# Performance work log

Measured on AMD Instinct MI355X. Metric: run time of the kernel, lower is better.

Reference implementation:

```python
import jax, jax.numpy as jnp
import numpy as np

A = 15                    # num_anchor_per_point
H = W = 34                # hardcoded feature map size in the torch module
STRIDE = 16               # heat_map_a
ANCHOR_W = jnp.array([45.3, 32.0, 22.6, 90.5, 64.0, 45.3, 181.0, 128.0, 90.5, 271.5, 192.0, 135.8, 362.0, 256.0, 181.0], dtype=jnp.float32)
ANCHOR_H = jnp.array([22.6, 32.0, 45.3, 45.3, 64.0, 90.5, 90.5, 128.0, 181.0, 135.8, 192.0, 271.5, 181.0, 256.0, 362.0], dtype=jnp.float32)
THRESH_OBJ = 0.2
MIN_H = 6.0
MIN_W = 6.0
MAX_CAND = 5000
TOP_N = 300
OVERLAP = 0.7


def _generate_anchors():
    xmins = -0.5 * (ANCHOR_W - 1.0)
    xmaxs = 0.5 * (ANCHOR_W - 1.0)
    ymins = -0.5 * (ANCHOR_H - 1.0)
    ymaxs = 0.5 * (ANCHOR_H - 1.0)
    return jnp.stack([xmins, ymins, xmaxs, ymaxs], axis=1)  # [A,4]


def _bbox_transform_inv(boxes, deltas):
    widths = boxes[:, 2] - boxes[:, 0] + 1.0
    heights = boxes[:, 3] - boxes[:, 1] + 1.0
    ctr_x = boxes[:, 0] + 0.5 * (widths - 1.0)
    ctr_y = boxes[:, 1] + 0.5 * (heights - 1.0)
    pred_ctr_x = deltas[:, 0] * widths + ctr_x
    pred_ctr_y = deltas[:, 1] * heights + ctr_y
    pred_w = jnp.exp(deltas[:, 2]) * widths
    pred_h = jnp.exp(deltas[:, 3]) * heights
    return jnp.stack([
        pred_ctr_x - 0.5 * (pred_w - 1.0),
        pred_ctr_y - 0.5 * (pred_h - 1.0),
        pred_ctr_x + 0.5 * (pred_w - 1.0),
        pred_ctr_y + 0.5 * (pred_h - 1.0),
    ], axis=1)


def _nms_keep(boxes, valid, thresh):
    # greedy NMS on score-descending boxes; +1 pixel convention matches module
    x1, y1, x2, y2 = boxes[:, 0], boxes[:, 1], boxes[:, 2], boxes[:, 3]
    areas = (x2 - x1 + 1.0) * (y2 - y1 + 1.0)
    iw = jnp.clip(jnp.minimum(x2[:, None], x2[None, :]) - jnp.maximum(x1[:, None], x1[None, :]) + 1.0, 0.0)
    ih = jnp.clip(jnp.minimum(y2[:, None], y2[None, :]) - jnp.maximum(y1[:, None], y1[None, :]) + 1.0, 0.0)
    inter = iw * ih
    iou = inter / (areas[:, None] + areas[None, :] - inter)  # [M,M]
    M = boxes.shape[0]
    idx = jnp.arange(M)

    def body(i, suppressed):
        alive = jnp.logical_not(suppressed[i])
        return suppressed | (alive & (iou[i] > thresh) & (idx > i))

    suppressed = jax.lax.fori_loop(0, M, body, jnp.logical_not(valid))
    return jnp.logical_not(suppressed) & valid


def _forward(rpn_cls_prob_reshape, rpn_bbox_pred, im_info, bbox_mean, bbox_std):
    origin_height = im_info[0].astype(jnp.float32)
    origin_width = im_info[1].astype(jnp.float32)

    # shifts (replicates torch meshgrid indexing='ij' and (y,x,y,x) column order)
    shift_x = jnp.arange(W, dtype=jnp.float32) * STRIDE
    shift_y = jnp.arange(H, dtype=jnp.float32) * STRIDE
    sx, sy = jnp.meshgrid(shift_x, shift_y, indexing='ij')  # [W,H]
    shifts = jnp.stack([sy.ravel(), sx.ravel(), sy.ravel(), sx.ravel()], axis=1)  # [W*H,4]
    anchors = (_generate_anchors()[None, :, :] + shifts[:, None, :]).reshape(-1, 4)  # [W*H*A,4]

    # deltas: [1,4A,34,34] -> (A,4,34,34) -> (34,34,A,4) -> (-1,4)
    deltas = rpn_bbox_pred.reshape(A, 4, H, W).transpose(2, 3, 0, 1).reshape(-1, 4)
    deltas = deltas * bbox_std + bbox_mean
    proposals = _bbox_transform_inv(anchors, deltas)

    # clip to image (refine_out_of_map_bbox=True)
    xs = jnp.clip(proposals[:, 0::2], 0.0, origin_width - 1.0)
    ys = jnp.clip(proposals[:, 1::2], 0.0, origin_height - 1.0)
    proposals = jnp.stack([xs[:, 0], ys[:, 0], xs[:, 1], ys[:, 1]], axis=1)

    # scores: [1,2A,34,34] -> (2,A,HW) -> (HW,A,2) -> (-1,2)
    scores = rpn_cls_prob_reshape.reshape(2, A, -1).transpose(2, 1, 0).reshape(-1, 2)

    # filter (HEIGHT_AND_WIDTH) via masking (jit-friendly, same selected set)
    ws = proposals[:, 2] - proposals[:, 0] + 1.0
    hs = proposals[:, 3] - proposals[:, 1] + 1.0
    keep = (scores[:, 1] > THRESH_OBJ) & (ws >= MIN_W) & (hs >= MIN_H)

    masked_score = jnp.where(keep, scores[:, 1], -1.0)
    top_vals, top_idx = jax.lax.top_k(masked_score, MAX_CAND)  # sorted descending
    cand = proposals[top_idx]
    valid = keep[top_idx]

    kept = _nms_keep(cand, valid, OVERLAP)

    # emit first TOP_N kept boxes in score order, zero-padded, with batch-id col 0
    rank = jnp.cumsum(kept.astype(jnp.int32)) - 1
    dest = jnp.where(kept & (rank < TOP_N), rank, TOP_N)
    out = jnp.zeros((TOP_N + 1, 5), dtype=cand.dtype)
    out = out.at[dest, 1:].set(cand)
    return out[:TOP_N]


def setup_inputs() -> dict:
    key = jax.random.key(0)
    k1, k2 = jax.random.split(key)
    rpn_cls_prob_reshape = jax.random.uniform(k1, (1, 2 * A, H, W), dtype=jnp.float32)
    rpn_bbox_pred = jax.random.normal(k2, (1, 4 * A, H, W), dtype=jnp.float32)
    im_info = jnp.array([544, 544], dtype=jnp.int32)
    bbox_mean = jnp.array([0.0, 0.0, 0.0, 0.0], dtype=jnp.float32)
    bbox_std = jnp.array([0.1, 0.1, 0.2, 0.2], dtype=jnp.float32)
    return {"rpn_cls_prob_reshape": rpn_cls_prob_reshape, "rpn_bbox_pred": rpn_bbox_pred,
            "im_info": im_info, "bbox_mean": bbox_mean, "bbox_std": bbox_std}


def reference(rpn_cls_prob_reshape, rpn_bbox_pred, im_info, bbox_mean, bbox_std):
    return _forward(rpn_cls_prob_reshape, rpn_bbox_pred, im_info, bbox_mean, bbox_std)
```

## Files before the change

kernel.cpp:

```cpp
#include <hip/hip_runtime.h>

#define NA 15
#define GH 34
#define GW 34
#define SP (GH*GW)
#define NB (SP*NA)
#define MAXC 5000
#define TOPN 300
#define NW 80
#define NRALLOC 5056
#define THRESH_OBJ 0.2f
#define NMS_T 0.7f
#define SH 12
#define BLO 0x3E4CCu
#define NBUCK 5120

typedef unsigned long long u64;
typedef unsigned int u32;
struct __align__(16) U2 { u64 x, y; };

__constant__ float c_aw[NA] = {45.3f,32.0f,22.6f,90.5f,64.0f,45.3f,181.0f,128.0f,90.5f,271.5f,192.0f,135.8f,362.0f,256.0f,181.0f};
__constant__ float c_ah[NA] = {22.6f,32.0f,45.3f,45.3f,64.0f,90.5f,90.5f,128.0f,181.0f,135.8f,192.0f,271.5f,181.0f,256.0f,362.0f};

__global__ __launch_bounds__(256) void k_decode(
    const float* __restrict__ cls, const float* __restrict__ pred,
    const int* __restrict__ iminfo, const float* __restrict__ mean,
    const float* __restrict__ stdv, float* __restrict__ boxes,
    u32* __restrict__ sbits) {
#pragma clang fp contract(off)
  int r = blockIdx.x * 256 + threadIdx.x;
  if (r >= NB) return;
  int n = r % NA;
  int p = r / NA;
  int w = p % GW;
  int h = p / GW;

  float score = cls[(NA + n) * SP + p];

  float d0 = pred[(n*4+0)*SP + p] * stdv[0] + mean[0];
  float d1 = pred[(n*4+1)*SP + p] * stdv[1] + mean[1];
  float d2 = pred[(n*4+2)*SP + p] * stdv[2] + mean[2];
  float d3 = pred[(n*4+3)*SP + p] * stdv[3] + mean[3];

  float aw = c_aw[n], ah = c_ah[n];
  float sx = (float)(w * 16);
  float sy = (float)(h * 16);
  float xmin = -0.5f * (aw - 1.0f) + sx;
  float ymin = -0.5f * (ah - 1.0f) + sy;
  float xmax =  0.5f * (aw - 1.0f) + sx;
  float ymax =  0.5f * (ah - 1.0f) + sy;

  float widths  = xmax - xmin + 1.0f;
  float heights = ymax - ymin + 1.0f;
  float ctrx = xmin + 0.5f * (widths - 1.0f);
  float ctry = ymin + 0.5f * (heights - 1.0f);

  float pcx = d0 * widths + ctrx;
  float pcy = d1 * heights + ctry;
  float pw = expf(d2) * widths;
  float ph = expf(d3) * heights;

  float x1 = pcx - 0.5f * (pw - 1.0f);
  float y1 = pcy - 0.5f * (ph - 1.0f);
  float x2 = pcx + 0.5f * (pw - 1.0f);
  float y2 = pcy + 0.5f * (ph - 1.0f);

  float ow = (float)iminfo[1] - 1.0f;
  float oh = (float)iminfo[0] - 1.0f;
  x1 = fminf(fmaxf(x1, 0.0f), ow);
  x2 = fminf(fmaxf(x2, 0.0f), ow);
  y1 = fminf(fmaxf(y1, 0.0f), oh);
  y2 = fminf(fmaxf(y2, 0.0f), oh);

  float ws = x2 - x1 + 1.0f;
  float hs = y2 - y1 + 1.0f;
  bool keep = (score > THRESH_OBJ) && (ws >= 6.0f) && (hs >= 6.0f);

  boxes[r*4+0] = x1;
  boxes[r*4+1] = y1;
  boxes[r*4+2] = x2;
  boxes[r*4+3] = y2;
  sbits[r] = keep ? __float_as_uint(score) : 0u;
}

__global__ __launch_bounds__(1024) void k_bucket(const u32* __restrict__ sbits,
    int* __restrict__ base, int* __restrict__ cnt, u64* __restrict__ blist) {
  __shared__ int sh[NBUCK];
  __shared__ int fl[NBUCK];
  __shared__ int ch[1024];
  int tid = threadIdx.x;
  for (int j = tid; j < NBUCK; j += 1024) { sh[j] = 0; fl[j] = 0; }
  __syncthreads();
  for (int j = tid; j < NB; j += 1024) {
    u32 bits = sbits[j];
    if (bits) { int b = min((int)((bits >> SH) - BLO), NBUCK - 1); atomicAdd(&sh[b], 1); }
  }
  __syncthreads();
  int c0 = sh[tid*5+0], c1 = sh[tid*5+1], c2 = sh[tid*5+2], c3 = sh[tid*5+3], c4 = sh[tid*5+4];
  ch[tid] = c0 + c1 + c2 + c3 + c4;
  __syncthreads();
  for (int off = 1; off < 1024; off <<= 1) {
    int v = ch[tid];
    int u = (tid + off < 1024) ? ch[tid + off] : 0;
    __syncthreads();
    ch[tid] = v + u;
    __syncthreads();
  }
  int S = (tid + 1 < 1024) ? ch[tid + 1] : 0;
  int b4v = S;
  int b3v = b4v + c4;
  int b2v = b3v + c3;
  int b1v = b2v + c2;
  int b0v = b1v + c1;
  base[tid*5+0] = b0v; base[tid*5+1] = b1v; base[tid*5+2] = b2v;
  base[tid*5+3] = b3v; base[tid*5+4] = b4v;
  sh[tid*5+0] = b0v; sh[tid*5+1] = b1v; sh[tid*5+2] = b2v;
  sh[tid*5+3] = b3v; sh[tid*5+4] = b4v;
  if (tid == 0) *cnt = ch[0];
  __syncthreads();
  for (int j = tid; j < NB; j += 1024) {
    u32 bits = sbits[j];
    if (!bits) continue;
    int b = min((int)((bits >> SH) - BLO), NBUCK - 1);
    int pos = sh[b] + atomicAdd(&fl[b], 1);
    blist[pos] = ((u64)bits << 32) | (u64)(0xFFFFFFFFu - (u32)j);
  }
}

__global__ __launch_bounds__(256) void k_final(const u32* __restrict__ sbits,
    const int* __restrict__ base, const int* __restrict__ cnt,
    const u64* __restrict__ blist, const float* __restrict__ boxes,
    float* __restrict__ sboxes) {
  int i = blockIdx.x * 256 + threadIdx.x;
  if (i >= NB) return;
  u32 bits = sbits[i];
  if (!bits) return;
  int b = min((int)((bits >> SH) - BLO), NBUCK - 1);
  u64 key = ((u64)bits << 32) | (u64)(0xFFFFFFFFu - (u32)i);
  int s = base[b];
  int e = (b > 0) ? base[b-1] : *cnt;
  int r = s;
  for (int p = s; p < e; ++p) r += (blist[p] > key) ? 1 : 0;
  if (r < MAXC) ((float4*)sboxes)[r] = ((const float4*)boxes)[i];
}

__global__ __launch_bounds__(64) void k_iou(const float* __restrict__ sboxes,
    const int* __restrict__ cnt, u64* __restrict__ mask) {
#pragma clang fp contract(off)
  int N = min(*cnt, MAXC);
  int bi = blockIdx.x, bj = blockIdx.y;
  if (bj < bi) return;
  int t = threadIdx.x;
  int i = bi * 64 + t;
  if (bi * 64 >= N) return;
  __shared__ float4 jb[64];
  int j0 = bj * 64;
  if (j0 + t < N) jb[t] = ((const float4*)sboxes)[j0 + t];
  __syncthreads();
  if (i >= N) return;
  float4 a = ((const float4*)sboxes)[i];
  float areaA = (a.z - a.x + 1.0f) * (a.w - a.y + 1.0f);
  u64 word = 0;
  int jmax = min(64, N - j0);
  for (int jj = 0; jj < jmax; ++jj) {
    int j = j0 + jj;
    if (j <= i) continue;
    float4 b = jb[jj];
    float iw = fminf(a.z, b.z) - fmaxf(a.x, b.x) + 1.0f;
    float ih = fminf(a.w, b.w) - fmaxf(a.y, b.y) + 1.0f;
    iw = fmaxf(iw, 0.0f);
    ih = fmaxf(ih, 0.0f);
    float inter = iw * ih;
    float areaB = (b.z - b.x + 1.0f) * (b.w - b.y + 1.0f);
    float iou = inter / (areaA + areaB - inter);
    if (iou > NMS_T) word |= (1ULL << jj);
  }
  mask[(size_t)i * NW + bj] = word;
}

__device__ __forceinline__ u64 rl64(u64 v, int l) {
  unsigned lo = __builtin_amdgcn_readlane((unsigned)(v & 0xffffffffULL), l);
  unsigned hi = __builtin_amdgcn_readlane((unsigned)(v >> 32), l);
  return ((u64)hi << 32) | (u64)lo;
}

__global__ __launch_bounds__(64, 1) void k_nms(const float* __restrict__ sboxes,
    const u64* __restrict__ mask, const int* __restrict__ cnt,
    float* __restrict__ out) {
  const int t = threadIdx.x;
  const int N = min(*cnt, MAXC);
  const int NBLK = (N + 63) >> 6;
  const int tt = (t < 40) ? t : 39;
  const bool lane_ok = (t < 40);
  const int w0i = 2 * tt, w1i = 2 * tt + 1;
  u64 rv0 = 0ULL, rv1 = 0ULL;
  __shared__ int klist[TOPN + 1];
  int kept = 0;

  u64 colA = 0ULL, colB = 0ULL;
  if (NBLK > 0) colA = mask[(size_t)t * NW + 0];

  for (int b = 0; b < NBLK; ++b) {
    u64 cc = (b & 1) ? colB : colA;
    int base = b * 64;
    u64 w = rl64((b & 1) ? rv1 : rv0, b >> 1);
    int nv = N - base; if (nv > 64) nv = 64;
    u64 valid = (nv >= 64) ? ~0ULL : ((1ULL << nv) - 1ULL);
    u64 avail = ~w & valid;
    int kept0 = kept;
    while (avail && kept < TOPN) {
#pragma unroll
      for (int u = 0; u < 4; ++u) {
        bool on = (avail != 0ULL) && (kept < TOPN);
        int d = (int)__builtin_ctzll(avail | (1ULL << 63));
        klist[on ? kept : TOPN] = base + d;
        u64 sup = rl64(cc, d);
        u64 clear = on ? (sup | (1ULL << d)) : 0ULL;
        avail &= ~clear;
        kept += on ? 1 : 0;
      }
    }
    if (kept >= TOPN) break;
    if (b + 1 < NBLK) {
      u64 nx = mask[(size_t)((b + 1) * 64 + t) * NW + (b + 1)];
      if (b & 1) colA = nx; else colB = nx;
    }
    int nk = kept - kept0;
    for (int c = 0; c < nk; c += 4) {
      int m = nk - c;
#define ROWK(K) int row##K = klist[(K < m) ? (kept0 + c + K) : 0];
      ROWK(0) ROWK(1) ROWK(2) ROWK(3)
#undef ROWK
#define LVK(K) U2 v##K = ((const U2*)(mask + (size_t)row##K * NW))[tt];
      LVK(0) LVK(1) LVK(2) LVK(3)
#undef LVK
      u64 o0 = 0, o1 = 0;
#define ACCK(K) { int bk = row##K >> 6; bool on = lane_ok && (K < m); \
      o0 |= (on && w0i >= bk) ? v##K.x : 0ULL; \
      o1 |= (on && w1i >= bk) ? v##K.y : 0ULL; }
      ACCK(0) ACCK(1) ACCK(2) ACCK(3)
#undef ACCK
      rv0 |= o0; rv1 |= o1;
    }
  }
  __syncthreads();
  for (int e = t; e < TOPN * 5; e += 64) {
    int row = e / 5, col = e % 5;
    float v = 0.0f;
    if (col > 0 && row < kept) v = sboxes[klist[row] * 4 + (col - 1)];
    out[e] = v;
  }
}

extern "C" void kernel_launch(void* const* d_in, const int* in_sizes, int n_in,
                              void* d_out, int out_size, void* d_ws, size_t ws_size,
                              hipStream_t stream) {
  const float* cls  = (const float*)d_in[0];
  const float* pred = (const float*)d_in[1];
  const int*   imi  = (const int*)d_in[2];
  const float* mean = (const float*)d_in[3];
  const float* stdv = (const float*)d_in[4];
  float* out = (float*)d_out;

  char* ws = (char*)d_ws;
  float* boxes  = (float*)(ws);
  u32*   sbits  = (u32*)(ws + 277440);
  float* sboxes = (float*)(ws + 346800);
  int*   cnt    = (int*)(ws + 426800);
  int*   base   = (int*)(ws + 426816);
  u64*   mask   = (u64*)(ws + 447296);
  u64*   blist  = mask;

  k_decode<<<(NB + 255) / 256, 256, 0, stream>>>(cls, pred, imi, mean, stdv, boxes, sbits);
  k_bucket<<<1, 1024, 0, stream>>>(sbits, base, cnt, blist);
  k_final<<<(NB + 255) / 256, 256, 0, stream>>>(sbits, base, cnt, blist, boxes, sboxes);
  dim3 giou((MAXC + 63) / 64, NW);
  k_iou<<<giou, 64, 0, stream>>>(sboxes, cnt, mask);
  k_nms<<<1, 64, 0, stream>>>(sboxes, mask, cnt, out);
}
```

Baseline: 111.2 us.

## Stream kept-row NMS masks into an LDS ring via async global_load_lds

In the single-wave NMS kernel, each kept box's suppression-mask row is now fetched with asynchronous global-to-LDS loads into an 8-slot ring while the serial ctz scan continues. The rows are OR-merged into the per-lane removal bits only when the ring fills, or at the start of the next 64-box block. Before, the scan ran first and the mask rows were loaded afterwards in groups of four. The aim is to hide global-memory latency behind the serial scan loop. In exchange it adds s_waitcnt stalls, extra LDS traffic and dependence on the global_load_lds builtin; the fallback path without that builtin would be incorrect.

```diff
diff --git a/kernel.cpp b/kernel.cpp
--- a/kernel.cpp
+++ b/kernel.cpp
@@ -184,6 +184,18 @@
   return ((u64)hi << 32) | (u64)lo;
 }
 
+__device__ __forceinline__ void gload_lds16(const void* g, void* l) {
+#if __has_builtin(__builtin_amdgcn_global_load_lds)
+  __builtin_amdgcn_global_load_lds(
+      (const __attribute__((address_space(1))) unsigned int*)g,
+      (__attribute__((address_space(3))) unsigned int*)l, 16, 0, 0);
+#else
+  U2 v = *(const U2*)g;
+  int t = threadIdx.x & 63;
+  *((U2*)l + 0) = v;
+#endif
+}
+
 __global__ __launch_bounds__(64, 1) void k_nms(const float* __restrict__ sboxes,
     const u64* __restrict__ mask, const int* __restrict__ cnt,
     float* __restrict__ out) {
@@ -194,55 +206,74 @@
   const bool lane_ok = (t < 40);
   const int w0i = 2 * tt, w1i = 2 * tt + 1;
   u64 rv0 = 0ULL, rv1 = 0ULL;
-  __shared__ int klist[TOPN + 1];
+  __shared__ int klist[TOPN + 8];
+  __shared__ u64 ring[8 * 128];
   int kept = 0;
 
   u64 colA = 0ULL, colB = 0ULL;
   if (NBLK > 0) colA = mask[(size_t)t * NW + 0];
 
+  int pslot = 0;
+  int pkbase = 0;
+
+#define MERGEK(K, nn) { int bk = r##K##_ >> 6; bool on = lane_ok && ((K) < (nn)); \
+    o0 |= (on && w0i >= bk) ? q##K.x : 0ULL; \
+    o1 |= (on && w1i >= bk) ? q##K.y : 0ULL; }
+#define FLUSHRING(n_, kb_) do { \
+    asm volatile("s_waitcnt vmcnt(0)" ::: "memory"); \
+    __builtin_amdgcn_sched_barrier(0); \
+    int nflush = (n_); int kb = (kb_); \
+    U2 q0 = *(const U2*)(ring + 0*128 + 2*tt); \
+    U2 q1 = *(const U2*)(ring + 1*128 + 2*tt); \
+    U2 q2 = *(const U2*)(ring + 2*128 + 2*tt); \
+    U2 q3 = *(const U2*)(ring + 3*128 + 2*tt); \
+    U2 q4 = *(const U2*)(ring + 4*128 + 2*tt); \
+    U2 q5 = *(const U2*)(ring + 5*128 + 2*tt); \
+    U2 q6 = *(const U2*)(ring + 6*128 + 2*tt); \
+    U2 q7 = *(const U2*)(ring + 7*128 + 2*tt); \
+    int r0_ = klist[kb+0], r1_ = klist[kb+1], r2_ = klist[kb+2], r3_ = klist[kb+3]; \
+    int r4_ = klist[kb+4], r5_ = klist[kb+5], r6_ = klist[kb+6], r7_ = klist[kb+7]; \
+    u64 o0 = 0, o1 = 0; \
+    MERGEK(0, nflush) MERGEK(1, nflush) MERGEK(2, nflush) MERGEK(3, nflush) \
+    MERGEK(4, nflush) MERGEK(5, nflush) MERGEK(6, nflush) MERGEK(7, nflush) \
+    rv0 |= o0; rv1 |= o1; \
+  } while (0)
+
   for (int b = 0; b < NBLK; ++b) {
     u64 cc = (b & 1) ? colB : colA;
+    if (pslot > 0) { FLUSHRING(pslot, pkbase); pslot = 0; }
     int base = b * 64;
     u64 w = rl64((b & 1) ? rv1 : rv0, b >> 1);
     int nv = N - base; if (nv > 64) nv = 64;
     u64 valid = (nv >= 64) ? ~0ULL : ((1ULL << nv) - 1ULL);
     u64 avail = ~w & valid;
-    int kept0 = kept;
-    while (avail && kept < TOPN) {
-#pragma unroll
-      for (int u = 0; u < 4; ++u) {
-        bool on = (avail != 0ULL) && (kept < TOPN);
-        int d = (int)__builtin_ctzll(avail | (1ULL << 63));
-        klist[on ? kept : TOPN] = base + d;
-        u64 sup = rl64(cc, d);
-        u64 clear = on ? (sup | (1ULL << d)) : 0ULL;
-        avail &= ~clear;
-        kept += on ? 1 : 0;
-      }
-    }
-    if (kept >= TOPN) break;
     if (b + 1 < NBLK) {
       u64 nx = mask[(size_t)((b + 1) * 64 + t) * NW + (b + 1)];
       if (b & 1) colA = nx; else colB = nx;
     }
-    int nk = kept - kept0;
-    for (int c = 0; c < nk; c += 4) {
-      int m = nk - c;
-#define ROWK(K) int row##K = klist[(K < m) ? (kept0 + c + K) : 0];
-      ROWK(0) ROWK(1) ROWK(2) ROWK(3)
-#undef ROWK
-#define LVK(K) U2 v##K = ((const U2*)(mask + (size_t)row##K * NW))[tt];
-      LVK(0) LVK(1) LVK(2) LVK(3)
-#undef LVK
-      u64 o0 = 0, o1 = 0;
-#define ACCK(K) { int bk = row##K >> 6; bool on = lane_ok && (K < m); \
-      o0 |= (on && w0i >= bk) ? v##K.x : 0ULL; \
-      o1 |= (on && w1i >= bk) ? v##K.y : 0ULL; }
-      ACCK(0) ACCK(1) ACCK(2) ACCK(3)
-#undef ACCK
-      rv0 |= o0; rv1 |= o1;
+    int kbase = kept;
+    int slot = 0;
+    while (avail) {
+      int d = (int)__builtin_ctzll(avail);
+      u64 sup = rl64(cc, d);
+      int row = base + d;
+      klist[kept] = row;
+      gload_lds16((const char*)(mask + (size_t)row * NW) + (size_t)tt * 16,
+                  (void*)(ring + (size_t)slot * 128));
+      avail &= ~(sup | (1ULL << d));
+      ++kept;
+      ++slot;
+      if (kept >= TOPN) goto scan_done;
+      if (slot == 8) {
+        FLUSHRING(8, kbase);
+        kbase += 8;
+        slot = 0;
+      }
     }
-  }
+    pslot = slot;
+    pkbase = kbase;
+  }
+scan_done:
   __syncthreads();
   for (int e = t; e < TOPN * 5; e += 64) {
     int row = e / 5, col = e % 5;
@@ -250,6 +281,8 @@
     if (col > 0 && row < kept) v = sboxes[klist[row] * 4 + (col - 1)];
     out[e] = v;
   }
+#undef FLUSHRING
+#undef MERGEK
 }
 
 extern "C" void kernel_launch(void* const* d_in, const int* in_sizes, int n_in,
```

Result: slower. 117.5 us (+5.7%).
